# Kernel tuning notes

Hardware: AMD Instinct MI355X
Metric: run time of the kernel (lower is better)

The kernel has to match this reference:

```python
import jax, jax.numpy as jnp
import numpy as np

K = 5              # kernel_size per pseudo dim
K3 = K ** 3        # 125 kernel weight slots
BITS = np.array([[(c >> d) & 1 for d in range(3)] for c in range(8)], dtype=np.int32)  # [8,3]
STRIDES = np.array([1, K, K * K], dtype=np.int32)

N0, E0 = 16384, 262144
N1, E1 = 4096, 65536
N2, E2 = 1024, 16384
N3, E3 = 256, 4096
B = 16
V = B * 8          # final dense 2x2x2 voxels per graph


def spline_conv(x, src, dst, pseudo, W, root, bias, num_nodes):
    """Degree-1 open B-spline conv (torch SplineConv, mean aggr + root + bias).
    x: [N,in], pseudo: [E,3] in [0,1], W: [K^3,in,out]."""
    v = pseudo * (K - 1)                         # [E,3]
    lo = jnp.clip(jnp.floor(v), 0, K - 2)
    frac = v - lo                                # [E,3]
    lo = lo.astype(jnp.int32)
    bits = jnp.asarray(BITS)                     # [8,3]
    idx = lo[:, None, :] + bits[None]            # [E,8,3]
    kidx = (idx * jnp.asarray(STRIDES)).sum(-1)  # [E,8] flat kernel index
    basis = jnp.where(bits[None].astype(bool), frac[:, None, :], 1.0 - frac[:, None, :]).prod(-1)  # [E,8]
    y = jnp.einsum('ni,kio->nko', x, W)          # [N,K3,out] per-node per-kernel transform
    yv = y[src[:, None], kidx]                   # [E,8,out] gather
    msg = (basis[..., None] * yv).sum(1)         # [E,out]
    agg = jax.ops.segment_sum(msg, dst, num_segments=num_nodes)
    deg = jax.ops.segment_sum(jnp.ones(dst.shape[0], x.dtype), dst, num_segments=num_nodes)
    agg = agg / jnp.maximum(deg, 1.0)[:, None]   # mean aggregation
    return agg + x @ root + bias


def pool_max(x, cluster, num_segments):
    p = jax.ops.segment_max(x, cluster, num_segments=num_segments)
    return jnp.where(jnp.isfinite(p), p, 0.0)    # empty voxels -> 0


def setup_inputs() -> dict:
    key = jax.random.key(0)
    ks = iter(jax.random.split(key, 64))
    f = lambda s, sc: jax.random.normal(next(ks), s, jnp.float32) * sc
    u = lambda s: jax.random.uniform(next(ks), s, jnp.float32)
    ri = lambda s, hi: jax.random.randint(next(ks), s, 0, hi, dtype=jnp.int32)
    return dict(
        x0=u((N0, 1)),
        pseudo0=u((E0, 3)), pseudo1=u((E1, 3)), pseudo2=u((E2, 3)), pseudo3=u((E3, 3)),
        W1=f((K3, 1, 32), 0.3), root1=f((1, 32), 0.3), b1=f((32,), 0.05),
        W2=f((K3, 32, 64), 0.05), root2=f((32, 64), 0.05), b2=f((64,), 0.05),
        W3=f((K3, 64, 64), 0.04), root3=f((64, 64), 0.04), b3=f((64,), 0.05),
        W4=f((K3, 64, 128), 0.04), root4=f((64, 128), 0.04), b4=f((128,), 0.05),
        fc1_w=f((1024, 256), 0.03), fc1_b=f((256,), 0.05),
        fc2_w=f((256, 10), 0.06), fc2_b=f((10,), 0.05),
        src0=ri((E0,), N0), dst0=ri((E0,), N0),
        src1=ri((E1,), N1), dst1=ri((E1,), N1),
        src2=ri((E2,), N2), dst2=ri((E2,), N2),
        src3=ri((E3,), N3), dst3=ri((E3,), N3),
        cluster0=ri((N0,), N1), cluster1=ri((N1,), N2),
        cluster2=ri((N2,), N3), cluster3=ri((N3,), V),
    )


def reference(x0, pseudo0, pseudo1, pseudo2, pseudo3,
              W1, root1, b1, W2, root2, b2, W3, root3, b3, W4, root4, b4,
              fc1_w, fc1_b, fc2_w, fc2_b,
              src0, dst0, src1, dst1, src2, dst2, src3, dst3,
              cluster0, cluster1, cluster2, cluster3):
    x = jax.nn.elu(spline_conv(x0, src0, dst0, pseudo0, W1, root1, b1, N0))
    x = pool_max(x, cluster0, N1)
    x = jax.nn.elu(spline_conv(x, src1, dst1, pseudo1, W2, root2, b2, N1))
    x = pool_max(x, cluster1, N2)
    x = jax.nn.elu(spline_conv(x, src2, dst2, pseudo2, W3, root3, b3, N2))
    x = pool_max(x, cluster2, N3)
    x = jax.nn.elu(spline_conv(x, src3, dst3, pseudo3, W4, root4, b4, N3))
    x = pool_max(x, cluster3, V)                 # [B*8, 128]
    x = x.reshape(B, 8 * 128)
    x = jax.nn.elu(x @ fc1_w + fc1_b)
    x = x @ fc2_w + fc2_b                        # dropout is a no-op in eval
    return jax.nn.log_softmax(x, axis=1)
```

## Files before the change

### kernel.cpp

```cpp
#include <hip/hip_runtime.h>
#include <hip/hip_bf16.h>
#include <math.h>

namespace {

typedef unsigned long long u64;
typedef __attribute__((ext_vector_type(8))) short bf16x8;
typedef __attribute__((ext_vector_type(4))) float f32x4;

constexpr int KK = 5;
constexpr int K3 = 125;
constexpr int N0 = 16384, E0 = 262144;
constexpr int N1 = 4096,  E1 = 65536;
constexpr int N2 = 1024,  E2 = 16384;
constexpr int N3 = 256,   E3 = 4096;
constexpr int NV = 128;
constexpr int E_TOT = E0 + E1 + E2 + E3;
constexpr unsigned ENC_NEG_INF = 0x007FFFFFu;

constexpr size_t A_PENC1 = 0;
constexpr size_t A_PENC2 = A_PENC1 + (size_t)N1 * 32;
constexpr size_t A_PENC3 = A_PENC2 + (size_t)N2 * 64;
constexpr size_t A_PENC4 = A_PENC3 + (size_t)N3 * 64;
constexpr size_t A_PENC_END = A_PENC4 + (size_t)NV * 128;
constexpr size_t PENC_TOTAL = A_PENC_END;

constexpr size_t A_WT2 = A_PENC_END;
constexpr size_t A_WT3 = A_WT2 + (size_t)K3 * 64 * 32 / 2;
constexpr size_t A_WT4 = A_WT3 + (size_t)K3 * 64 * 64 / 2;

constexpr size_t A_BAS0 = A_WT4 + (size_t)K3 * 128 * 64 / 2;
constexpr size_t A_KID0 = A_BAS0 + (size_t)E0 * 8;
constexpr size_t A_BAS1 = A_KID0 + (size_t)E0 * 2;
constexpr size_t A_KID1 = A_BAS1 + (size_t)E1 * 8;
constexpr size_t A_BAS2 = A_KID1 + (size_t)E1 * 2;
constexpr size_t A_KID2 = A_BAS2 + (size_t)E2 * 8;
constexpr size_t A_BAS3 = A_KID2 + (size_t)E2 * 2;
constexpr size_t A_KID3 = A_BAS3 + (size_t)E3 * 8;

constexpr size_t A_OFF0 = A_KID3 + (size_t)E3 * 2;
constexpr size_t A_OFF1 = A_OFF0 + (N0 + 4);
constexpr size_t A_OFF2 = A_OFF1 + (N1 + 4);
constexpr size_t A_OFF3 = A_OFF2 + (N2 + 4);
constexpr size_t A_CUR0 = A_OFF3 + (N3 + 4);
constexpr size_t A_CUR1 = A_CUR0 + N0;
constexpr size_t A_CUR2 = A_CUR1 + N1;
constexpr size_t A_CUR3 = A_CUR2 + N2;
constexpr size_t A_CUR_END = A_CUR3 + N3;
constexpr size_t CUR_TOTAL = A_CUR_END - A_CUR0;
constexpr size_t A_EIX0 = A_CUR_END;
constexpr size_t A_EIX1 = A_EIX0 + E0;
constexpr size_t A_EIX2 = A_EIX1 + E1;
constexpr size_t A_EIX3 = A_EIX2 + E2;
constexpr size_t A_Y = A_EIX3 + E3;
constexpr size_t Y_FLOATS = (size_t)N1 * (K3 * 64) / 2;
constexpr size_t A_FCP = A_Y + Y_FLOATS;

__device__ __forceinline__ float eluf(float x) { return x > 0.f ? x : expm1f(x); }

__device__ __forceinline__ unsigned enc_f(float x) {
    unsigned u = __float_as_uint(x);
    return (u & 0x80000000u) ? ~u : (u | 0x80000000u);
}
__device__ __forceinline__ float dec_fin(unsigned u) {
    u = (u & 0x80000000u) ? (u & 0x7fffffffu) : ~u;
    float v = __uint_as_float(u);
    return isfinite(v) ? v : 0.f;
}
__device__ __forceinline__ float bf2f(unsigned short u) {
    return __uint_as_float((unsigned)u << 16);
}
__device__ __forceinline__ unsigned short f2bf(float v) {
    __hip_bfloat16 h = __float2bfloat16(v);
    return *reinterpret_cast<unsigned short*>(&h);
}

__device__ __forceinline__ void decode_edge(const float* __restrict__ pseudo, int e,
                                            float bas[8], int kid[8]) {
    float v0 = pseudo[e * 3 + 0] * (KK - 1);
    float v1 = pseudo[e * 3 + 1] * (KK - 1);
    float v2 = pseudo[e * 3 + 2] * (KK - 1);
    float f0 = fminf(fmaxf(floorf(v0), 0.f), (float)(KK - 2));
    float f1 = fminf(fmaxf(floorf(v1), 0.f), (float)(KK - 2));
    float f2 = fminf(fmaxf(floorf(v2), 0.f), (float)(KK - 2));
    int lo0 = (int)f0, lo1 = (int)f1, lo2 = (int)f2;
    float fr0 = v0 - f0, fr1 = v1 - f1, fr2 = v2 - f2;
#pragma unroll
    for (int c = 0; c < 8; ++c) {
        int b0 = c & 1, b1 = (c >> 1) & 1, b2 = (c >> 2) & 1;
        kid[c] = (lo0 + b0) + (lo1 + b1) * KK + (lo2 + b2) * KK * KK;
        bas[c] = (b0 ? fr0 : 1.f - fr0) * (b1 ? fr1 : 1.f - fr1) * (b2 ? fr2 : 1.f - fr2);
    }
}

__global__ void prologue1(const float* __restrict__ ps0, const float* __restrict__ ps1,
                          const float* __restrict__ ps2, const float* __restrict__ ps3,
                          const int* __restrict__ d0, const int* __restrict__ d1,
                          const int* __restrict__ d2, const int* __restrict__ d3,
                          float* __restrict__ ws) {
    int g = blockIdx.x * blockDim.x + threadIdx.x;
    if (g < (int)PENC_TOTAL) ((unsigned*)(ws + A_PENC1))[g] = ENC_NEG_INF;
    if (g >= E_TOT) return;
    const float* ps; float* bas; u64* kid; int e; const int* dst; int* cur;
    if (g < E0)                { ps = ps0; bas = ws + A_BAS0; kid = (u64*)(ws + A_KID0); e = g;                dst = d0; cur = (int*)(ws + A_CUR0); }
    else if (g < E0 + E1)      { ps = ps1; bas = ws + A_BAS1; kid = (u64*)(ws + A_KID1); e = g - E0;           dst = d1; cur = (int*)(ws + A_CUR1); }
    else if (g < E0 + E1 + E2) { ps = ps2; bas = ws + A_BAS2; kid = (u64*)(ws + A_KID2); e = g - E0 - E1;      dst = d2; cur = (int*)(ws + A_CUR2); }
    else                       { ps = ps3; bas = ws + A_BAS3; kid = (u64*)(ws + A_KID3); e = g - E0 - E1 - E2; dst = d3; cur = (int*)(ws + A_CUR3); }
    atomicAdd(&cur[dst[e]], 1);
    float b[8]; int k[8];
    decode_edge(ps, e, b, k);
    *(float4*)(bas + (size_t)e * 8)     = make_float4(b[0], b[1], b[2], b[3]);
    *(float4*)(bas + (size_t)e * 8 + 4) = make_float4(b[4], b[5], b[6], b[7]);
    u64 p = 0;
#pragma unroll
    for (int c = 0; c < 8; ++c) p |= (u64)(unsigned)k[c] << (8 * c);
    kid[e] = p;
}

__global__ void csr_scan(float* __restrict__ ws) {
    __shared__ int ls[1024];
    int* cur; int* off; int N;
    switch (blockIdx.x) {
        case 0:  cur = (int*)(ws + A_CUR0); off = (int*)(ws + A_OFF0); N = N0; break;
        case 1:  cur = (int*)(ws + A_CUR1); off = (int*)(ws + A_OFF1); N = N1; break;
        case 2:  cur = (int*)(ws + A_CUR2); off = (int*)(ws + A_OFF2); N = N2; break;
        default: cur = (int*)(ws + A_CUR3); off = (int*)(ws + A_OFF3); N = N3; break;
    }
    int t = threadIdx.x;
    int chunk = (N + 1023) >> 10;
    int b0 = t * chunk;
    int b1 = min(b0 + chunk, N);
    int s = 0;
    for (int i = b0; i < b1; ++i) s += cur[i];
    ls[t] = s;
    __syncthreads();
    for (int d = 1; d < 1024; d <<= 1) {
        int v = (t >= d) ? ls[t - d] : 0;
        __syncthreads();
        ls[t] += v;
        __syncthreads();
    }
    int run = (t == 0) ? 0 : ls[t - 1];
    for (int i = b0; i < b1; ++i) {
        int c = cur[i];
        off[i] = run;
        cur[i] = run;
        run += c;
    }
    if (t == 1023) off[N] = run;
}

__global__ void prologue4(const int* __restrict__ d0, const int* __restrict__ d1,
                          const int* __restrict__ d2, const int* __restrict__ d3,
                          const float* __restrict__ W2, const float* __restrict__ W3,
                          const float* __restrict__ W4, float* __restrict__ ws) {
    __shared__ float st[64 * 129];
    int bid = blockIdx.x;
    int tid = threadIdx.x;
    if (bid < 3 * K3) {
        const float* W; unsigned short* wt; int IN, OUT, k;
        if (bid < K3)          { W = W2; wt = (unsigned short*)(ws + A_WT2); IN = 32; OUT = 64;  k = bid; }
        else if (bid < 2 * K3) { W = W3; wt = (unsigned short*)(ws + A_WT3); IN = 64; OUT = 64;  k = bid - K3; }
        else                   { W = W4; wt = (unsigned short*)(ws + A_WT4); IN = 64; OUT = 128; k = bid - 2 * K3; }
        int tot = IN * OUT;
        const float* Wk = W + (size_t)k * tot;
        for (int idx = tid; idx < tot; idx += 256) {
            int i = idx / OUT, o = idx % OUT;
            st[i * (OUT + 1) + o] = Wk[idx];
        }
        __syncthreads();
        unsigned short* wk = wt + (size_t)k * tot;
        for (int idx = tid; idx < tot; idx += 256) {
            int o = idx / IN, i = idx % IN;
            wk[idx] = f2bf(st[i * (OUT + 1) + o]);
        }
    } else {
        int g = (bid - 3 * K3) * 256 + tid;
        if (g < E0)                { int p = atomicAdd((int*)(ws + A_CUR0) + d0[g], 1);            ((int*)(ws + A_EIX0))[p] = g; }
        else if (g < E0 + E1)      { int e = g - E0;           int p = atomicAdd((int*)(ws + A_CUR1) + d1[e], 1); ((int*)(ws + A_EIX1))[p] = e; }
        else if (g < E0 + E1 + E2) { int e = g - E0 - E1;      int p = atomicAdd((int*)(ws + A_CUR2) + d2[e], 1); ((int*)(ws + A_EIX2))[p] = e; }
        else if (g < E_TOT)        { int e = g - E0 - E1 - E2; int p = atomicAdd((int*)(ws + A_CUR3) + d3[e], 1); ((int*)(ws + A_EIX3))[p] = e; }
    }
}

__global__ __launch_bounds__(256) void l1_agg(const float* __restrict__ x0,
                                              const float* __restrict__ bas,
                                              const u64* __restrict__ kid,
                                              const int* __restrict__ src,
                                              const int* __restrict__ off,
                                              const int* __restrict__ eidx,
                                              const float* __restrict__ W1,
                                              const float* __restrict__ root1,
                                              const float* __restrict__ b1,
                                              const int* __restrict__ cl,
                                              unsigned* __restrict__ penc) {
    __shared__ float wlds[K3 * 32];
    int tid = threadIdx.x;
    for (int i = tid; i < K3 * 32; i += 256) wlds[i] = W1[i];
    __syncthreads();
    int o = tid & 31;
    int nsub = tid >> 5;
    int n = blockIdx.x * 8 + nsub;
    int s0 = off[n], s1 = off[n + 1];
    float acc = 0.f;
    int j = s0;
    for (; j + 2 <= s1; j += 2) {
        int ea = eidx[j], eb = eidx[j + 1];
        float4 qa0 = *(const float4*)(bas + (size_t)ea * 8);
        float4 qa1 = *(const float4*)(bas + (size_t)ea * 8 + 4);
        float4 qb0 = *(const float4*)(bas + (size_t)eb * 8);
        float4 qb1 = *(const float4*)(bas + (size_t)eb * 8 + 4);
        u64 ka = kid[ea], kb = kid[eb];
        float xa = x0[src[ea]], xb = x0[src[eb]];
        float ma, mb;
        ma  = qa0.x * wlds[((int)( ka        & 255u)) * 32 + o];
        ma += qa0.y * wlds[((int)((ka >>  8) & 255u)) * 32 + o];
        ma += qa0.z * wlds[((int)((ka >> 16) & 255u)) * 32 + o];
        ma += qa0.w * wlds[((int)((ka >> 24) & 255u)) * 32 + o];
        ma += qa1.x * wlds[((int)((ka >> 32) & 255u)) * 32 + o];
        ma += qa1.y * wlds[((int)((ka >> 40) & 255u)) * 32 + o];
        ma += qa1.z * wlds[((int)((ka >> 48) & 255u)) * 32 + o];
        ma += qa1.w * wlds[((int)((ka >> 56) & 255u)) * 32 + o];
        mb  = qb0.x * wlds[((int)( kb        & 255u)) * 32 + o];
        mb += qb0.y * wlds[((int)((kb >>  8) & 255u)) * 32 + o];
        mb += qb0.z * wlds[((int)((kb >> 16) & 255u)) * 32 + o];
        mb += qb0.w * wlds[((int)((kb >> 24) & 255u)) * 32 + o];
        mb += qb1.x * wlds[((int)((kb >> 32) & 255u)) * 32 + o];
        mb += qb1.y * wlds[((int)((kb >> 40) & 255u)) * 32 + o];
        mb += qb1.z * wlds[((int)((kb >> 48) & 255u)) * 32 + o];
        mb += qb1.w * wlds[((int)((kb >> 56) & 255u)) * 32 + o];
        acc = fmaf(xa, ma, fmaf(xb, mb, acc));
    }
    if (j < s1) {
        int e = eidx[j];
        float4 q0 = *(const float4*)(bas + (size_t)e * 8);
        float4 q1 = *(const float4*)(bas + (size_t)e * 8 + 4);
        u64 k8 = kid[e];
        float xv = x0[src[e]];
        float m;
        m  = q0.x * wlds[((int)( k8        & 255u)) * 32 + o];
        m += q0.y * wlds[((int)((k8 >>  8) & 255u)) * 32 + o];
        m += q0.z * wlds[((int)((k8 >> 16) & 255u)) * 32 + o];
        m += q0.w * wlds[((int)((k8 >> 24) & 255u)) * 32 + o];
        m += q1.x * wlds[((int)((k8 >> 32) & 255u)) * 32 + o];
        m += q1.y * wlds[((int)((k8 >> 40) & 255u)) * 32 + o];
        m += q1.z * wlds[((int)((k8 >> 48) & 255u)) * 32 + o];
        m += q1.w * wlds[((int)((k8 >> 56) & 255u)) * 32 + o];
        acc = fmaf(xv, m, acc);
    }
    float dg = fmaxf((float)(s1 - s0), 1.f);
    float val = acc / dg + x0[n] * root1[o] + b1[o];
    val = eluf(val);
    atomicMax(&penc[(size_t)cl[n] * 32 + o], enc_f(val));
}

template <int IN>
__global__ __launch_bounds__(256) void gemm_y_mfma(const unsigned* __restrict__ penc,
                                                   const unsigned short* __restrict__ wt,
                                                   unsigned short* __restrict__ y,
                                                   int N, int KO) {
    int wid = (blockIdx.x * 256 + threadIdx.x) >> 6;
    int lane = threadIdx.x & 63;
    int nTiles = N >> 4;
    int n0 = (wid % nTiles) << 4;
    int ko0 = (wid / nTiles) << 6;
    int l15 = lane & 15;
    int kk = (lane >> 4) << 3;

    f32x4 acc[4];
#pragma unroll
    for (int t = 0; t < 4; ++t) acc[t] = (f32x4){0.f, 0.f, 0.f, 0.f};

#pragma unroll
    for (int s = 0; s < IN / 32; ++s) {
        const unsigned* pp = penc + (size_t)(n0 + l15) * IN + s * 32 + kk;
        uint4 u0 = *(const uint4*)pp;
        uint4 u1 = *(const uint4*)(pp + 4);
        unsigned uu[8] = {u0.x, u0.y, u0.z, u0.w, u1.x, u1.y, u1.z, u1.w};
        bf16x8 bfrag;
#pragma unroll
        for (int t = 0; t < 8; ++t) bfrag[t] = (short)f2bf(dec_fin(uu[t]));
#pragma unroll
        for (int t = 0; t < 4; ++t) {
            bf16x8 afrag = *(const bf16x8*)(wt + (size_t)(ko0 + t * 16 + l15) * IN + s * 32 + kk);
            acc[t] = __builtin_amdgcn_mfma_f32_16x16x32_bf16(afrag, bfrag, acc[t], 0, 0, 0);
        }
    }
    int rbase = (lane >> 4) << 2;
#pragma unroll
    for (int t = 0; t < 4; ++t) {
        ushort4 sv;
        sv.x = f2bf(acc[t][0]);
        sv.y = f2bf(acc[t][1]);
        sv.z = f2bf(acc[t][2]);
        sv.w = f2bf(acc[t][3]);
        *(ushort4*)(y + (size_t)(n0 + l15) * KO + ko0 + t * 16 + rbase) = sv;
    }
}

template <int IN, int OUT>
__global__ __launch_bounds__(256) void gather_agg(const unsigned short* __restrict__ y,
                                                  const float* __restrict__ bas,
                                                  const u64* __restrict__ kid,
                                                  const int* __restrict__ src,
                                                  const int* __restrict__ off,
                                                  const int* __restrict__ eidx,
                                                  const unsigned* __restrict__ penc_prev,
                                                  const float* __restrict__ root,
                                                  const float* __restrict__ bias,
                                                  const int* __restrict__ cl,
                                                  unsigned* __restrict__ penc) {
    constexpr int KO = K3 * OUT;
    constexpr int WPT = OUT / 64;
    int lane = threadIdx.x & 63;
    int wv = threadIdx.x >> 6;
    int n = blockIdx.x * 4 + wv;
    int s0 = off[n], s1 = off[n + 1];
    float acc0 = 0.f, acc1 = 0.f;
    int j = s0;
    for (; j + 2 <= s1; j += 2) {
        int ea = eidx[j], eb = eidx[j + 1];
        float4 qa0 = *(const float4*)(bas + (size_t)ea * 8);
        float4 qa1 = *(const float4*)(bas + (size_t)ea * 8 + 4);
        float4 qb0 = *(const float4*)(bas + (size_t)eb * 8);
        float4 qb1 = *(const float4*)(bas + (size_t)eb * 8 + 4);
        u64 ka = kid[ea], kb = kid[eb];
        const unsigned short* ypa = y + (size_t)src[ea] * KO + lane;
        const unsigned short* ypb = y + (size_t)src[eb] * KO + lane;
        float ba[8] = {qa0.x, qa0.y, qa0.z, qa0.w, qa1.x, qa1.y, qa1.z, qa1.w};
        float bb[8] = {qb0.x, qb0.y, qb0.z, qb0.w, qb1.x, qb1.y, qb1.z, qb1.w};
        float va[8], vb[8], va2[8], vb2[8];
#pragma unroll
        for (int c = 0; c < 8; ++c) {
            int kca = (int)((ka >> (8 * c)) & 255u);
            int kcb = (int)((kb >> (8 * c)) & 255u);
            va[c] = bf2f(ypa[(size_t)kca * OUT]);
            vb[c] = bf2f(ypb[(size_t)kcb * OUT]);
            if (WPT == 2) {
                va2[c] = bf2f(ypa[(size_t)kca * OUT + 64]);
                vb2[c] = bf2f(ypb[(size_t)kcb * OUT + 64]);
            }
        }
#pragma unroll
        for (int c = 0; c < 8; ++c) {
            acc0 = fmaf(ba[c], va[c], acc0);
            acc0 = fmaf(bb[c], vb[c], acc0);
            if (WPT == 2) {
                acc1 = fmaf(ba[c], va2[c], acc1);
                acc1 = fmaf(bb[c], vb2[c], acc1);
            }
        }
    }
    if (j < s1) {
        int e = eidx[j];
        float4 q0 = *(const float4*)(bas + (size_t)e * 8);
        float4 q1 = *(const float4*)(bas + (size_t)e * 8 + 4);
        u64 k8 = kid[e];
        const unsigned short* yp = y + (size_t)src[e] * KO + lane;
        float b[8] = {q0.x, q0.y, q0.z, q0.w, q1.x, q1.y, q1.z, q1.w};
#pragma unroll
        for (int c = 0; c < 8; ++c) {
            int kc = (int)((k8 >> (8 * c)) & 255u);
            acc0 = fmaf(b[c], bf2f(yp[(size_t)kc * OUT]), acc0);
            if (WPT == 2) acc1 = fmaf(b[c], bf2f(yp[(size_t)kc * OUT + 64]), acc1);
        }
    }
    float dg = fmaxf((float)(s1 - s0), 1.f);
    float accs[2] = {acc0, acc1};
#pragma unroll
    for (int w = 0; w < WPT; ++w) {
        int o = lane + 64 * w;
        float r = 0.f;
        for (int i = 0; i < IN; ++i)
            r = fmaf(dec_fin(penc_prev[(size_t)n * IN + i]), root[(size_t)i * OUT + o], r);
        float val = accs[w] / dg + r + bias[o];
        val = eluf(val);
        atomicMax(&penc[(size_t)cl[n] * OUT + o], enc_f(val));
    }
}

__global__ __launch_bounds__(256) void fc1_part(const unsigned* __restrict__ penc4,
                                                const float* __restrict__ w1,
                                                float* __restrict__ part) {
    __shared__ float xs[64];
    int ks = blockIdx.x & 15;
    int bq = blockIdx.x >> 4;
    int t = threadIdx.x;
    int k0 = ks * 64;
    if (t < 64) xs[t] = dec_fin(penc4[(size_t)bq * 1024 + k0 + t]);
    __syncthreads();
    const float* wp = w1 + (size_t)k0 * 256 + t;
    float acc = 0.f;
#pragma unroll 8
    for (int k = 0; k < 64; ++k)
        acc = fmaf(xs[k], wp[(size_t)k * 256], acc);
    part[((size_t)bq * 16 + ks) * 256 + t] = acc;
}

__global__ __launch_bounds__(256) void fc_head2(const float* __restrict__ part,
                                                const float* __restrict__ b1,
                                                const float* __restrict__ w2,
                                                const float* __restrict__ b2,
                                                float* __restrict__ out) {
    __shared__ float h[256];
    __shared__ float l[10];
    __shared__ float red[2];
    int bq = blockIdx.x;
    int t = threadIdx.x;
    const float* pp = part + (size_t)bq * 16 * 256 + t;
    float acc = b1[t];
#pragma unroll
    for (int ks = 0; ks < 16; ++ks) acc += pp[ks * 256];
    h[t] = eluf(acc);
    __syncthreads();
    if (t < 10) {
        float a2 = b2[t];
        for (int q = 0; q < 256; ++q)
            a2 = fmaf(h[q], w2[(size_t)q * 10 + t], a2);
        l[t] = a2;
    }
    __syncthreads();
    if (t == 0) {
        float m = l[0];
        for (int i = 1; i < 10; ++i) m = fmaxf(m, l[i]);
        float s = 0.f;
        for (int i = 0; i < 10; ++i) s += expf(l[i] - m);
        red[0] = m;
        red[1] = logf(s);
    }
    __syncthreads();
    if (t < 10) out[(size_t)bq * 10 + t] = l[t] - red[0] - red[1];
}

inline unsigned blk(long long t) { return (unsigned)((t + 255) / 256); }

}

extern "C" void kernel_launch(void* const* d_in, const int* in_sizes, int n_in,
                              void* d_out, int out_size, void* d_ws, size_t ws_size,
                              hipStream_t stream) {
    const float* x0    = (const float*)d_in[0];
    const float* ps0   = (const float*)d_in[1];
    const float* ps1   = (const float*)d_in[2];
    const float* ps2   = (const float*)d_in[3];
    const float* ps3   = (const float*)d_in[4];
    const float* W1    = (const float*)d_in[5];
    const float* root1 = (const float*)d_in[6];
    const float* b1    = (const float*)d_in[7];
    const float* W2    = (const float*)d_in[8];
    const float* root2 = (const float*)d_in[9];
    const float* b2    = (const float*)d_in[10];
    const float* W3    = (const float*)d_in[11];
    const float* root3 = (const float*)d_in[12];
    const float* b3    = (const float*)d_in[13];
    const float* W4    = (const float*)d_in[14];
    const float* root4 = (const float*)d_in[15];
    const float* b4    = (const float*)d_in[16];
    const float* fc1w  = (const float*)d_in[17];
    const float* fc1b  = (const float*)d_in[18];
    const float* fc2w  = (const float*)d_in[19];
    const float* fc2b  = (const float*)d_in[20];
    const int* src0 = (const int*)d_in[21];
    const int* dst0 = (const int*)d_in[22];
    const int* src1 = (const int*)d_in[23];
    const int* dst1 = (const int*)d_in[24];
    const int* src2 = (const int*)d_in[25];
    const int* dst2 = (const int*)d_in[26];
    const int* src3 = (const int*)d_in[27];
    const int* dst3 = (const int*)d_in[28];
    const int* cl0  = (const int*)d_in[29];
    const int* cl1  = (const int*)d_in[30];
    const int* cl2  = (const int*)d_in[31];
    const int* cl3  = (const int*)d_in[32];

    float* ws = (float*)d_ws;
    float* out = (float*)d_out;

    unsigned* penc1 = (unsigned*)(ws + A_PENC1);
    unsigned* penc2 = (unsigned*)(ws + A_PENC2);
    unsigned* penc3 = (unsigned*)(ws + A_PENC3);
    unsigned* penc4 = (unsigned*)(ws + A_PENC4);
    unsigned short* wt2 = (unsigned short*)(ws + A_WT2);
    unsigned short* wt3 = (unsigned short*)(ws + A_WT3);
    unsigned short* wt4 = (unsigned short*)(ws + A_WT4);
    float* bas0 = ws + A_BAS0;  u64* kid0 = (u64*)(ws + A_KID0);
    float* bas1 = ws + A_BAS1;  u64* kid1 = (u64*)(ws + A_KID1);
    float* bas2 = ws + A_BAS2;  u64* kid2 = (u64*)(ws + A_KID2);
    float* bas3 = ws + A_BAS3;  u64* kid3 = (u64*)(ws + A_KID3);
    int* off0 = (int*)(ws + A_OFF0);  int* eix0 = (int*)(ws + A_EIX0);
    int* off1 = (int*)(ws + A_OFF1);  int* eix1 = (int*)(ws + A_EIX1);
    int* off2 = (int*)(ws + A_OFF2);  int* eix2 = (int*)(ws + A_EIX2);
    int* off3 = (int*)(ws + A_OFF3);  int* eix3 = (int*)(ws + A_EIX3);
    unsigned short* yb = (unsigned short*)(ws + A_Y);
    float* fcp = ws + A_FCP;

    hipMemsetAsync(ws + A_CUR0, 0, CUR_TOTAL * sizeof(int), stream);
    prologue1<<<blk(E_TOT), 256, 0, stream>>>(ps0, ps1, ps2, ps3, dst0, dst1, dst2, dst3, ws);
    csr_scan<<<4, 1024, 0, stream>>>(ws);
    prologue4<<<3 * K3 + blk(E_TOT), 256, 0, stream>>>(dst0, dst1, dst2, dst3, W2, W3, W4, ws);

    l1_agg<<<N0 / 8, 256, 0, stream>>>(x0, bas0, kid0, src0, off0, eix0, W1, root1, b1, cl0, penc1);

    gemm_y_mfma<32><<<(N1 / 16) * (K3 * 64 / 64) / 4, 256, 0, stream>>>(penc1, wt2, yb, N1, K3 * 64);
    gather_agg<32, 64><<<N1 / 4, 256, 0, stream>>>(yb, bas1, kid1, src1, off1, eix1,
                                                   penc1, root2, b2, cl1, penc2);

    gemm_y_mfma<64><<<(N2 / 16) * (K3 * 64 / 64) / 4, 256, 0, stream>>>(penc2, wt3, yb, N2, K3 * 64);
    gather_agg<64, 64><<<N2 / 4, 256, 0, stream>>>(yb, bas2, kid2, src2, off2, eix2,
                                                   penc2, root3, b3, cl2, penc3);

    gemm_y_mfma<64><<<(N3 / 16) * (K3 * 128 / 64) / 4, 256, 0, stream>>>(penc3, wt4, yb, N3, K3 * 128);
    gather_agg<64, 128><<<N3 / 4, 256, 0, stream>>>(yb, bas3, kid3, src3, off3, eix3,
                                                    penc3, root4, b4, cl3, penc4);

    fc1_part<<<16 * 16, 256, 0, stream>>>(penc4, fc1w, fcp);
    fc_head2<<<16, 256, 0, stream>>>(fcp, fc1b, fc2w, fc2b, out);
}
```

Measured before the change: 346.8 us.

## Fuse all phases into one persistent cooperative kernel with grid syncs

Replaces the chain of a dozen separate kernel launches with a single cooperative persistent kernel that runs every phase in grid-stride loops, separated by grid-wide barriers, and keeps the multi-launch path as a fallback. It also shrinks the CSR scan to 256 threads and splits the weight transpose into 32-row halves so one shared buffer serves all phases. The aim is to remove per-launch overhead and the gaps between dependent small kernels. In exchange, the grid is capped by occupancy, so large phases get fewer blocks and each grid.sync adds its own cost.

```diff
diff --git a/kernel.cpp b/kernel.cpp
--- a/kernel.cpp
+++ b/kernel.cpp
@@ -1,6 +1,9 @@
 #include <hip/hip_runtime.h>
+#include <hip/hip_cooperative_groups.h>
 #include <hip/hip_bf16.h>
 #include <math.h>
+
+namespace cg = cooperative_groups;
 
 namespace {
 
@@ -14,15 +17,15 @@
 constexpr int N1 = 4096,  E1 = 65536;
 constexpr int N2 = 1024,  E2 = 16384;
 constexpr int N3 = 256,   E3 = 4096;
-constexpr int NV = 128;
 constexpr int E_TOT = E0 + E1 + E2 + E3;
 constexpr unsigned ENC_NEG_INF = 0x007FFFFFu;
+constexpr int KO2 = K3 * 64, KO3 = K3 * 64, KO4 = K3 * 128;
 
 constexpr size_t A_PENC1 = 0;
 constexpr size_t A_PENC2 = A_PENC1 + (size_t)N1 * 32;
 constexpr size_t A_PENC3 = A_PENC2 + (size_t)N2 * 64;
 constexpr size_t A_PENC4 = A_PENC3 + (size_t)N3 * 64;
-constexpr size_t A_PENC_END = A_PENC4 + (size_t)NV * 128;
+constexpr size_t A_PENC_END = A_PENC4 + (size_t)128 * 128;
 constexpr size_t PENC_TOTAL = A_PENC_END;
 
 constexpr size_t A_WT2 = A_PENC_END;
@@ -53,8 +56,20 @@
 constexpr size_t A_EIX2 = A_EIX1 + E1;
 constexpr size_t A_EIX3 = A_EIX2 + E2;
 constexpr size_t A_Y = A_EIX3 + E3;
-constexpr size_t Y_FLOATS = (size_t)N1 * (K3 * 64) / 2;
+constexpr size_t Y_FLOATS = (size_t)N1 * KO2 / 2;
 constexpr size_t A_FCP = A_Y + Y_FLOATS;
+
+constexpr int SMEM_FLOATS = 4128;
+
+struct P {
+    const float *x0, *W1, *root1, *b1, *root2, *b2, *root3, *b3, *root4, *b4;
+    const float *ps0, *ps1, *ps2, *ps3;
+    const float *W2, *W3, *W4, *fc1w, *fc1b, *fc2w, *fc2b;
+    const int *src0, *dst0, *src1, *dst1, *src2, *dst2, *src3, *dst3;
+    const int *cl0, *cl1, *cl2, *cl3;
+    float* ws;
+    float* out;
+};
 
 __device__ __forceinline__ float eluf(float x) { return x > 0.f ? x : expm1f(x); }
 
@@ -93,426 +108,488 @@
     }
 }
 
-__global__ void prologue1(const float* __restrict__ ps0, const float* __restrict__ ps1,
-                          const float* __restrict__ ps2, const float* __restrict__ ps3,
-                          const int* __restrict__ d0, const int* __restrict__ d1,
-                          const int* __restrict__ d2, const int* __restrict__ d3,
-                          float* __restrict__ ws) {
-    int g = blockIdx.x * blockDim.x + threadIdx.x;
-    if (g < (int)PENC_TOTAL) ((unsigned*)(ws + A_PENC1))[g] = ENC_NEG_INF;
-    if (g >= E_TOT) return;
-    const float* ps; float* bas; u64* kid; int e; const int* dst; int* cur;
-    if (g < E0)                { ps = ps0; bas = ws + A_BAS0; kid = (u64*)(ws + A_KID0); e = g;                dst = d0; cur = (int*)(ws + A_CUR0); }
-    else if (g < E0 + E1)      { ps = ps1; bas = ws + A_BAS1; kid = (u64*)(ws + A_KID1); e = g - E0;           dst = d1; cur = (int*)(ws + A_CUR1); }
-    else if (g < E0 + E1 + E2) { ps = ps2; bas = ws + A_BAS2; kid = (u64*)(ws + A_KID2); e = g - E0 - E1;      dst = d2; cur = (int*)(ws + A_CUR2); }
-    else                       { ps = ps3; bas = ws + A_BAS3; kid = (u64*)(ws + A_KID3); e = g - E0 - E1 - E2; dst = d3; cur = (int*)(ws + A_CUR3); }
-    atomicAdd(&cur[dst[e]], 1);
-    float b[8]; int k[8];
-    decode_edge(ps, e, b, k);
-    *(float4*)(bas + (size_t)e * 8)     = make_float4(b[0], b[1], b[2], b[3]);
-    *(float4*)(bas + (size_t)e * 8 + 4) = make_float4(b[4], b[5], b[6], b[7]);
-    u64 p = 0;
-#pragma unroll
-    for (int c = 0; c < 8; ++c) p |= (u64)(unsigned)k[c] << (8 * c);
-    kid[e] = p;
-}
-
-__global__ void csr_scan(float* __restrict__ ws) {
-    __shared__ int ls[1024];
-    int* cur; int* off; int N;
-    switch (blockIdx.x) {
-        case 0:  cur = (int*)(ws + A_CUR0); off = (int*)(ws + A_OFF0); N = N0; break;
-        case 1:  cur = (int*)(ws + A_CUR1); off = (int*)(ws + A_OFF1); N = N1; break;
-        case 2:  cur = (int*)(ws + A_CUR2); off = (int*)(ws + A_OFF2); N = N2; break;
-        default: cur = (int*)(ws + A_CUR3); off = (int*)(ws + A_OFF3); N = N3; break;
-    }
-    int t = threadIdx.x;
-    int chunk = (N + 1023) >> 10;
-    int b0 = t * chunk;
-    int b1 = min(b0 + chunk, N);
-    int s = 0;
-    for (int i = b0; i < b1; ++i) s += cur[i];
-    ls[t] = s;
+__device__ void ph0(const P& p) {
+    float* ws = p.ws;
+    for (int g = blockIdx.x * 256 + threadIdx.x; g < E_TOT; g += gridDim.x * 256) {
+        if (g < (int)PENC_TOTAL) ((unsigned*)(ws + A_PENC1))[g] = ENC_NEG_INF;
+        const float* ps; float* bas; u64* kid; int e; const int* dst; int* cur;
+        if (g < E0)                { ps = p.ps0; bas = ws + A_BAS0; kid = (u64*)(ws + A_KID0); e = g;                dst = p.dst0; cur = (int*)(ws + A_CUR0); }
+        else if (g < E0 + E1)      { ps = p.ps1; bas = ws + A_BAS1; kid = (u64*)(ws + A_KID1); e = g - E0;           dst = p.dst1; cur = (int*)(ws + A_CUR1); }
+        else if (g < E0 + E1 + E2) { ps = p.ps2; bas = ws + A_BAS2; kid = (u64*)(ws + A_KID2); e = g - E0 - E1;      dst = p.dst2; cur = (int*)(ws + A_CUR2); }
+        else                       { ps = p.ps3; bas = ws + A_BAS3; kid = (u64*)(ws + A_KID3); e = g - E0 - E1 - E2; dst = p.dst3; cur = (int*)(ws + A_CUR3); }
+        atomicAdd(&cur[dst[e]], 1);
+        float b[8]; int k[8];
+        decode_edge(ps, e, b, k);
+        *(float4*)(bas + (size_t)e * 8)     = make_float4(b[0], b[1], b[2], b[3]);
+        *(float4*)(bas + (size_t)e * 8 + 4) = make_float4(b[4], b[5], b[6], b[7]);
+        u64 pk = 0;
+#pragma unroll
+        for (int c = 0; c < 8; ++c) pk |= (u64)(unsigned)k[c] << (8 * c);
+        kid[e] = pk;
+    }
+}
+
+__device__ void ph1(const P& p, float* smem) {
+    float* ws = p.ws;
+    if (blockIdx.x < 4) {
+        int* ls = (int*)smem;
+        int* cur; int* off; int N;
+        switch (blockIdx.x) {
+            case 0:  cur = (int*)(ws + A_CUR0); off = (int*)(ws + A_OFF0); N = N0; break;
+            case 1:  cur = (int*)(ws + A_CUR1); off = (int*)(ws + A_OFF1); N = N1; break;
+            case 2:  cur = (int*)(ws + A_CUR2); off = (int*)(ws + A_OFF2); N = N2; break;
+            default: cur = (int*)(ws + A_CUR3); off = (int*)(ws + A_OFF3); N = N3; break;
+        }
+        int t = threadIdx.x;
+        int chunk = N >> 8;
+        int b0 = t * chunk, b1 = b0 + chunk;
+        int s = 0;
+        for (int i = b0; i < b1; ++i) s += cur[i];
+        ls[t] = s;
+        __syncthreads();
+        for (int d = 1; d < 256; d <<= 1) {
+            int v = (t >= d) ? ls[t - d] : 0;
+            __syncthreads();
+            ls[t] += v;
+            __syncthreads();
+        }
+        int run = (t == 0) ? 0 : ls[t - 1];
+        for (int i = b0; i < b1; ++i) {
+            int c = cur[i];
+            off[i] = run;
+            cur[i] = run;
+            run += c;
+        }
+        if (t == 255) off[N] = run;
+    }
+}
+
+__device__ void ph2(const P& p, float* smem) {
+    float* ws = p.ws;
+    constexpr int NW = 3 * K3;
+    constexpr int NS = E_TOT / 256;
+    for (int u = blockIdx.x; u < NW + NS; u += gridDim.x) {
+        if (u < NW) {
+            const float* W; unsigned short* wt; int IN, OUT, k;
+            if (u < K3)          { W = p.W2; wt = (unsigned short*)(ws + A_WT2); IN = 32; OUT = 64;  k = u; }
+            else if (u < 2 * K3) { W = p.W3; wt = (unsigned short*)(ws + A_WT3); IN = 64; OUT = 64;  k = u - K3; }
+            else                 { W = p.W4; wt = (unsigned short*)(ws + A_WT4); IN = 64; OUT = 128; k = u - 2 * K3; }
+            const float* Wk = W + (size_t)k * IN * OUT;
+            unsigned short* wk = wt + (size_t)k * IN * OUT;
+            int halves = IN / 32;
+            for (int h = 0; h < halves; ++h) {
+                __syncthreads();
+                for (int idx = threadIdx.x; idx < 32 * OUT; idx += 256) {
+                    int i2 = idx / OUT, o = idx % OUT;
+                    smem[i2 * (OUT + 1) + o] = Wk[(size_t)(h * 32 + i2) * OUT + o];
+                }
+                __syncthreads();
+                for (int idx = threadIdx.x; idx < OUT * 32; idx += 256) {
+                    int o = idx / 32, i2 = idx % 32;
+                    wk[(size_t)o * IN + h * 32 + i2] = f2bf(smem[i2 * (OUT + 1) + o]);
+                }
+            }
+        } else {
+            int g = (u - NW) * 256 + threadIdx.x;
+            if (g < E0)                { int q = atomicAdd((int*)(ws + A_CUR0) + p.dst0[g], 1);            ((int*)(ws + A_EIX0))[q] = g; }
+            else if (g < E0 + E1)      { int e = g - E0;           int q = atomicAdd((int*)(ws + A_CUR1) + p.dst1[e], 1); ((int*)(ws + A_EIX1))[q] = e; }
+            else if (g < E0 + E1 + E2) { int e = g - E0 - E1;      int q = atomicAdd((int*)(ws + A_CUR2) + p.dst2[e], 1); ((int*)(ws + A_EIX2))[q] = e; }
+            else                       { int e = g - E0 - E1 - E2; int q = atomicAdd((int*)(ws + A_CUR3) + p.dst3[e], 1); ((int*)(ws + A_EIX3))[q] = e; }
+        }
+    }
+}
+
+__device__ void ph3(const P& p, float* smem) {
+    float* ws = p.ws;
+    float* wlds = smem;
+    for (int i = threadIdx.x; i < K3 * 32; i += 256) wlds[i] = p.W1[i];
     __syncthreads();
-    for (int d = 1; d < 1024; d <<= 1) {
-        int v = (t >= d) ? ls[t - d] : 0;
-        __syncthreads();
-        ls[t] += v;
-        __syncthreads();
-    }
-    int run = (t == 0) ? 0 : ls[t - 1];
-    for (int i = b0; i < b1; ++i) {
-        int c = cur[i];
-        off[i] = run;
-        cur[i] = run;
-        run += c;
-    }
-    if (t == 1023) off[N] = run;
-}
-
-__global__ void prologue4(const int* __restrict__ d0, const int* __restrict__ d1,
-                          const int* __restrict__ d2, const int* __restrict__ d3,
-                          const float* __restrict__ W2, const float* __restrict__ W3,
-                          const float* __restrict__ W4, float* __restrict__ ws) {
-    __shared__ float st[64 * 129];
-    int bid = blockIdx.x;
-    int tid = threadIdx.x;
-    if (bid < 3 * K3) {
-        const float* W; unsigned short* wt; int IN, OUT, k;
-        if (bid < K3)          { W = W2; wt = (unsigned short*)(ws + A_WT2); IN = 32; OUT = 64;  k = bid; }
-        else if (bid < 2 * K3) { W = W3; wt = (unsigned short*)(ws + A_WT3); IN = 64; OUT = 64;  k = bid - K3; }
-        else                   { W = W4; wt = (unsigned short*)(ws + A_WT4); IN = 64; OUT = 128; k = bid - 2 * K3; }
-        int tot = IN * OUT;
-        const float* Wk = W + (size_t)k * tot;
-        for (int idx = tid; idx < tot; idx += 256) {
-            int i = idx / OUT, o = idx % OUT;
-            st[i * (OUT + 1) + o] = Wk[idx];
-        }
-        __syncthreads();
-        unsigned short* wk = wt + (size_t)k * tot;
-        for (int idx = tid; idx < tot; idx += 256) {
-            int o = idx / IN, i = idx % IN;
-            wk[idx] = f2bf(st[i * (OUT + 1) + o]);
-        }
-    } else {
-        int g = (bid - 3 * K3) * 256 + tid;
-        if (g < E0)                { int p = atomicAdd((int*)(ws + A_CUR0) + d0[g], 1);            ((int*)(ws + A_EIX0))[p] = g; }
-        else if (g < E0 + E1)      { int e = g - E0;           int p = atomicAdd((int*)(ws + A_CUR1) + d1[e], 1); ((int*)(ws + A_EIX1))[p] = e; }
-        else if (g < E0 + E1 + E2) { int e = g - E0 - E1;      int p = atomicAdd((int*)(ws + A_CUR2) + d2[e], 1); ((int*)(ws + A_EIX2))[p] = e; }
-        else if (g < E_TOT)        { int e = g - E0 - E1 - E2; int p = atomicAdd((int*)(ws + A_CUR3) + d3[e], 1); ((int*)(ws + A_EIX3))[p] = e; }
-    }
-}
-
-__global__ __launch_bounds__(256) void l1_agg(const float* __restrict__ x0,
-                                              const float* __restrict__ bas,
-                                              const u64* __restrict__ kid,
-                                              const int* __restrict__ src,
-                                              const int* __restrict__ off,
-                                              const int* __restrict__ eidx,
-                                              const float* __restrict__ W1,
-                                              const float* __restrict__ root1,
-                                              const float* __restrict__ b1,
-                                              const int* __restrict__ cl,
-                                              unsigned* __restrict__ penc) {
-    __shared__ float wlds[K3 * 32];
-    int tid = threadIdx.x;
-    for (int i = tid; i < K3 * 32; i += 256) wlds[i] = W1[i];
-    __syncthreads();
-    int o = tid & 31;
-    int nsub = tid >> 5;
-    int n = blockIdx.x * 8 + nsub;
-    int s0 = off[n], s1 = off[n + 1];
-    float acc = 0.f;
-    int j = s0;
-    for (; j + 2 <= s1; j += 2) {
-        int ea = eidx[j], eb = eidx[j + 1];
-        float4 qa0 = *(const float4*)(bas + (size_t)ea * 8);
-        float4 qa1 = *(const float4*)(bas + (size_t)ea * 8 + 4);
-        float4 qb0 = *(const float4*)(bas + (size_t)eb * 8);
-        float4 qb1 = *(const float4*)(bas + (size_t)eb * 8 + 4);
-        u64 ka = kid[ea], kb = kid[eb];
-        float xa = x0[src[ea]], xb = x0[src[eb]];
-        float ma, mb;
-        ma  = qa0.x * wlds[((int)( ka        & 255u)) * 32 + o];
-        ma += qa0.y * wlds[((int)((ka >>  8) & 255u)) * 32 + o];
-        ma += qa0.z * wlds[((int)((ka >> 16) & 255u)) * 32 + o];
-        ma += qa0.w * wlds[((int)((ka >> 24) & 255u)) * 32 + o];
-        ma += qa1.x * wlds[((int)((ka >> 32) & 255u)) * 32 + o];
-        ma += qa1.y * wlds[((int)((ka >> 40) & 255u)) * 32 + o];
-        ma += qa1.z * wlds[((int)((ka >> 48) & 255u)) * 32 + o];
-        ma += qa1.w * wlds[((int)((ka >> 56) & 255u)) * 32 + o];
-        mb  = qb0.x * wlds[((int)( kb        & 255u)) * 32 + o];
-        mb += qb0.y * wlds[((int)((kb >>  8) & 255u)) * 32 + o];
-        mb += qb0.z * wlds[((int)((kb >> 16) & 255u)) * 32 + o];
-        mb += qb0.w * wlds[((int)((kb >> 24) & 255u)) * 32 + o];
-        mb += qb1.x * wlds[((int)((kb >> 32) & 255u)) * 32 + o];
-        mb += qb1.y * wlds[((int)((kb >> 40) & 255u)) * 32 + o];
-        mb += qb1.z * wlds[((int)((kb >> 48) & 255u)) * 32 + o];
-        mb += qb1.w * wlds[((int)((kb >> 56) & 255u)) * 32 + o];
-        acc = fmaf(xa, ma, fmaf(xb, mb, acc));
-    }
-    if (j < s1) {
-        int e = eidx[j];
-        float4 q0 = *(const float4*)(bas + (size_t)e * 8);
-        float4 q1 = *(const float4*)(bas + (size_t)e * 8 + 4);
-        u64 k8 = kid[e];
-        float xv = x0[src[e]];
-        float m;
-        m  = q0.x * wlds[((int)( k8        & 255u)) * 32 + o];
-        m += q0.y * wlds[((int)((k8 >>  8) & 255u)) * 32 + o];
-        m += q0.z * wlds[((int)((k8 >> 16) & 255u)) * 32 + o];
-        m += q0.w * wlds[((int)((k8 >> 24) & 255u)) * 32 + o];
-        m += q1.x * wlds[((int)((k8 >> 32) & 255u)) * 32 + o];
-        m += q1.y * wlds[((int)((k8 >> 40) & 255u)) * 32 + o];
-        m += q1.z * wlds[((int)((k8 >> 48) & 255u)) * 32 + o];
-        m += q1.w * wlds[((int)((k8 >> 56) & 255u)) * 32 + o];
-        acc = fmaf(xv, m, acc);
-    }
-    float dg = fmaxf((float)(s1 - s0), 1.f);
-    float val = acc / dg + x0[n] * root1[o] + b1[o];
-    val = eluf(val);
-    atomicMax(&penc[(size_t)cl[n] * 32 + o], enc_f(val));
+    const float* bas = ws + A_BAS0;
+    const u64* kid = (const u64*)(ws + A_KID0);
+    const int* off = (const int*)(ws + A_OFF0);
+    const int* eidx = (const int*)(ws + A_EIX0);
+    unsigned* penc = (unsigned*)(ws + A_PENC1);
+    int o = threadIdx.x & 31;
+    int nsub = threadIdx.x >> 5;
+    for (int nb = blockIdx.x; nb < N0 / 8; nb += gridDim.x) {
+        int n = nb * 8 + nsub;
+        int s0 = off[n], s1 = off[n + 1];
+        float acc = 0.f;
+        int j = s0;
+        for (; j + 2 <= s1; j += 2) {
+            int ea = eidx[j], eb = eidx[j + 1];
+            float4 qa0 = *(const float4*)(bas + (size_t)ea * 8);
+            float4 qa1 = *(const float4*)(bas + (size_t)ea * 8 + 4);
+            float4 qb0 = *(const float4*)(bas + (size_t)eb * 8);
+            float4 qb1 = *(const float4*)(bas + (size_t)eb * 8 + 4);
+            u64 ka = kid[ea], kb = kid[eb];
+            float xa = p.x0[p.src0[ea]], xb = p.x0[p.src0[eb]];
+            float ma, mb;
+            ma  = qa0.x * wlds[((int)( ka        & 255u)) * 32 + o];
+            ma += qa0.y * wlds[((int)((ka >>  8) & 255u)) * 32 + o];
+            ma += qa0.z * wlds[((int)((ka >> 16) & 255u)) * 32 + o];
+            ma += qa0.w * wlds[((int)((ka >> 24) & 255u)) * 32 + o];
+            ma += qa1.x * wlds[((int)((ka >> 32) & 255u)) * 32 + o];
+            ma += qa1.y * wlds[((int)((ka >> 40) & 255u)) * 32 + o];
+            ma += qa1.z * wlds[((int)((ka >> 48) & 255u)) * 32 + o];
+            ma += qa1.w * wlds[((int)((ka >> 56) & 255u)) * 32 + o];
+            mb  = qb0.x * wlds[((int)( kb        & 255u)) * 32 + o];
+            mb += qb0.y * wlds[((int)((kb >>  8) & 255u)) * 32 + o];
+            mb += qb0.z * wlds[((int)((kb >> 16) & 255u)) * 32 + o];
+            mb += qb0.w * wlds[((int)((kb >> 24) & 255u)) * 32 + o];
+            mb += qb1.x * wlds[((int)((kb >> 32) & 255u)) * 32 + o];
+            mb += qb1.y * wlds[((int)((kb >> 40) & 255u)) * 32 + o];
+            mb += qb1.z * wlds[((int)((kb >> 48) & 255u)) * 32 + o];
+            mb += qb1.w * wlds[((int)((kb >> 56) & 255u)) * 32 + o];
+            acc = fmaf(xa, ma, fmaf(xb, mb, acc));
+        }
+        if (j < s1) {
+            int e = eidx[j];
+            float4 q0 = *(const float4*)(bas + (size_t)e * 8);
+            float4 q1 = *(const float4*)(bas + (size_t)e * 8 + 4);
+            u64 k8 = kid[e];
+            float xv = p.x0[p.src0[e]];
+            float m;
+            m  = q0.x * wlds[((int)( k8        & 255u)) * 32 + o];
+            m += q0.y * wlds[((int)((k8 >>  8) & 255u)) * 32 + o];
+            m += q0.z * wlds[((int)((k8 >> 16) & 255u)) * 32 + o];
+            m += q0.w * wlds[((int)((k8 >> 24) & 255u)) * 32 + o];
+            m += q1.x * wlds[((int)((k8 >> 32) & 255u)) * 32 + o];
+            m += q1.y * wlds[((int)((k8 >> 40) & 255u)) * 32 + o];
+            m += q1.z * wlds[((int)((k8 >> 48) & 255u)) * 32 + o];
+            m += q1.w * wlds[((int)((k8 >> 56) & 255u)) * 32 + o];
+            acc = fmaf(xv, m, acc);
+        }
+        float dg = fmaxf((float)(s1 - s0), 1.f);
+        float val = acc / dg + p.x0[n] * p.root1[o] + p.b1[o];
+        val = eluf(val);
+        atomicMax(&penc[(size_t)p.cl0[n] * 32 + o], enc_f(val));
+    }
 }
 
 template <int IN>
-__global__ __launch_bounds__(256) void gemm_y_mfma(const unsigned* __restrict__ penc,
-                                                   const unsigned short* __restrict__ wt,
-                                                   unsigned short* __restrict__ y,
-                                                   int N, int KO) {
-    int wid = (blockIdx.x * 256 + threadIdx.x) >> 6;
+__device__ void ph_gemm(const unsigned* __restrict__ penc,
+                        const unsigned short* __restrict__ wt,
+                        unsigned short* __restrict__ y, int N, int KO) {
     int lane = threadIdx.x & 63;
+    int wsub = threadIdx.x >> 6;
     int nTiles = N >> 4;
-    int n0 = (wid % nTiles) << 4;
-    int ko0 = (wid / nTiles) << 6;
+    int totalU = nTiles * (KO / 64) / 4;
     int l15 = lane & 15;
     int kk = (lane >> 4) << 3;
-
-    f32x4 acc[4];
-#pragma unroll
-    for (int t = 0; t < 4; ++t) acc[t] = (f32x4){0.f, 0.f, 0.f, 0.f};
-
-#pragma unroll
-    for (int s = 0; s < IN / 32; ++s) {
-        const unsigned* pp = penc + (size_t)(n0 + l15) * IN + s * 32 + kk;
-        uint4 u0 = *(const uint4*)pp;
-        uint4 u1 = *(const uint4*)(pp + 4);
-        unsigned uu[8] = {u0.x, u0.y, u0.z, u0.w, u1.x, u1.y, u1.z, u1.w};
-        bf16x8 bfrag;
-#pragma unroll
-        for (int t = 0; t < 8; ++t) bfrag[t] = (short)f2bf(dec_fin(uu[t]));
+    int rbase = (lane >> 4) << 2;
+    for (int u = blockIdx.x; u < totalU; u += gridDim.x) {
+        int wid = u * 4 + wsub;
+        int n0 = (wid % nTiles) << 4;
+        int ko0 = (wid / nTiles) << 6;
+        f32x4 acc[4];
+#pragma unroll
+        for (int t = 0; t < 4; ++t) acc[t] = (f32x4){0.f, 0.f, 0.f, 0.f};
+#pragma unroll
+        for (int s = 0; s < IN / 32; ++s) {
+            const unsigned* pp = penc + (size_t)(n0 + l15) * IN + s * 32 + kk;
+            uint4 u0 = *(const uint4*)pp;
+            uint4 u1 = *(const uint4*)(pp + 4);
+            unsigned uu[8] = {u0.x, u0.y, u0.z, u0.w, u1.x, u1.y, u1.z, u1.w};
+            bf16x8 bfrag;
+#pragma unroll
+            for (int t = 0; t < 8; ++t) bfrag[t] = (short)f2bf(dec_fin(uu[t]));
+#pragma unroll
+            for (int t = 0; t < 4; ++t) {
+                bf16x8 afrag = *(const bf16x8*)(wt + (size_t)(ko0 + t * 16 + l15) * IN + s * 32 + kk);
+                acc[t] = __builtin_amdgcn_mfma_f32_16x16x32_bf16(afrag, bfrag, acc[t], 0, 0, 0);
+            }
+        }
 #pragma unroll
         for (int t = 0; t < 4; ++t) {
-            bf16x8 afrag = *(const bf16x8*)(wt + (size_t)(ko0 + t * 16 + l15) * IN + s * 32 + kk);
-            acc[t] = __builtin_amdgcn_mfma_f32_16x16x32_bf16(afrag, bfrag, acc[t], 0, 0, 0);
-        }
-    }
-    int rbase = (lane >> 4) << 2;
-#pragma unroll
-    for (int t = 0; t < 4; ++t) {
-        ushort4 sv;
-        sv.x = f2bf(acc[t][0]);
-        sv.y = f2bf(acc[t][1]);
-        sv.z = f2bf(acc[t][2]);
-        sv.w = f2bf(acc[t][3]);
-        *(ushort4*)(y + (size_t)(n0 + l15) * KO + ko0 + t * 16 + rbase) = sv;
+            ushort4 sv;
+            sv.x = f2bf(acc[t][0]);
+            sv.y = f2bf(acc[t][1]);
+            sv.z = f2bf(acc[t][2]);
+            sv.w = f2bf(acc[t][3]);
+            *(ushort4*)(y + (size_t)(n0 + l15) * KO + ko0 + t * 16 + rbase) = sv;
+        }
     }
 }
 
 template <int IN, int OUT>
-__global__ __launch_bounds__(256) void gather_agg(const unsigned short* __restrict__ y,
-                                                  const float* __restrict__ bas,
-                                                  const u64* __restrict__ kid,
-                                                  const int* __restrict__ src,
-                                                  const int* __restrict__ off,
-                                                  const int* __restrict__ eidx,
-                                                  const unsigned* __restrict__ penc_prev,
-                                                  const float* __restrict__ root,
-                                                  const float* __restrict__ bias,
-                                                  const int* __restrict__ cl,
-                                                  unsigned* __restrict__ penc) {
+__device__ void ph_gather(const unsigned short* __restrict__ y,
+                          const float* __restrict__ bas,
+                          const u64* __restrict__ kid,
+                          const int* __restrict__ src,
+                          const int* __restrict__ off,
+                          const int* __restrict__ eidx,
+                          const unsigned* __restrict__ penc_prev,
+                          const float* __restrict__ root,
+                          const float* __restrict__ bias,
+                          const int* __restrict__ cl,
+                          unsigned* __restrict__ penc, int N) {
     constexpr int KO = K3 * OUT;
     constexpr int WPT = OUT / 64;
     int lane = threadIdx.x & 63;
     int wv = threadIdx.x >> 6;
-    int n = blockIdx.x * 4 + wv;
-    int s0 = off[n], s1 = off[n + 1];
-    float acc0 = 0.f, acc1 = 0.f;
-    int j = s0;
-    for (; j + 2 <= s1; j += 2) {
-        int ea = eidx[j], eb = eidx[j + 1];
-        float4 qa0 = *(const float4*)(bas + (size_t)ea * 8);
-        float4 qa1 = *(const float4*)(bas + (size_t)ea * 8 + 4);
-        float4 qb0 = *(const float4*)(bas + (size_t)eb * 8);
-        float4 qb1 = *(const float4*)(bas + (size_t)eb * 8 + 4);
-        u64 ka = kid[ea], kb = kid[eb];
-        const unsigned short* ypa = y + (size_t)src[ea] * KO + lane;
-        const unsigned short* ypb = y + (size_t)src[eb] * KO + lane;
-        float ba[8] = {qa0.x, qa0.y, qa0.z, qa0.w, qa1.x, qa1.y, qa1.z, qa1.w};
-        float bb[8] = {qb0.x, qb0.y, qb0.z, qb0.w, qb1.x, qb1.y, qb1.z, qb1.w};
-        float va[8], vb[8], va2[8], vb2[8];
-#pragma unroll
-        for (int c = 0; c < 8; ++c) {
-            int kca = (int)((ka >> (8 * c)) & 255u);
-            int kcb = (int)((kb >> (8 * c)) & 255u);
-            va[c] = bf2f(ypa[(size_t)kca * OUT]);
-            vb[c] = bf2f(ypb[(size_t)kcb * OUT]);
-            if (WPT == 2) {
-                va2[c] = bf2f(ypa[(size_t)kca * OUT + 64]);
-                vb2[c] = bf2f(ypb[(size_t)kcb * OUT + 64]);
+    for (int u = blockIdx.x; u < N / 4; u += gridDim.x) {
+        int n = u * 4 + wv;
+        int s0 = off[n], s1 = off[n + 1];
+        float acc0 = 0.f, acc1 = 0.f;
+        int j = s0;
+        for (; j + 2 <= s1; j += 2) {
+            int ea = eidx[j], eb = eidx[j + 1];
+            float4 qa0 = *(const float4*)(bas + (size_t)ea * 8);
+            float4 qa1 = *(const float4*)(bas + (size_t)ea * 8 + 4);
+            float4 qb0 = *(const float4*)(bas + (size_t)eb * 8);
+            float4 qb1 = *(const float4*)(bas + (size_t)eb * 8 + 4);
+            u64 ka = kid[ea], kb = kid[eb];
+            const unsigned short* ypa = y + (size_t)src[ea] * KO + lane;
+            const unsigned short* ypb = y + (size_t)src[eb] * KO + lane;
+            float ba[8] = {qa0.x, qa0.y, qa0.z, qa0.w, qa1.x, qa1.y, qa1.z, qa1.w};
+            float bb[8] = {qb0.x, qb0.y, qb0.z, qb0.w, qb1.x, qb1.y, qb1.z, qb1.w};
+            float va[8], vb[8], va2[8], vb2[8];
+#pragma unroll
+            for (int c = 0; c < 8; ++c) {
+                int kca = (int)((ka >> (8 * c)) & 255u);
+                int kcb = (int)((kb >> (8 * c)) & 255u);
+                va[c] = bf2f(ypa[(size_t)kca * OUT]);
+                vb[c] = bf2f(ypb[(size_t)kcb * OUT]);
+                if (WPT == 2) {
+                    va2[c] = bf2f(ypa[(size_t)kca * OUT + 64]);
+                    vb2[c] = bf2f(ypb[(size_t)kcb * OUT + 64]);
+                }
             }
-        }
-#pragma unroll
-        for (int c = 0; c < 8; ++c) {
-            acc0 = fmaf(ba[c], va[c], acc0);
-            acc0 = fmaf(bb[c], vb[c], acc0);
-            if (WPT == 2) {
-                acc1 = fmaf(ba[c], va2[c], acc1);
-                acc1 = fmaf(bb[c], vb2[c], acc1);
+#pragma unroll
+            for (int c = 0; c < 8; ++c) {
+                acc0 = fmaf(ba[c], va[c], acc0);
+                acc0 = fmaf(bb[c], vb[c], acc0);
+                if (WPT == 2) {
+                    acc1 = fmaf(ba[c], va2[c], acc1);
+                    acc1 = fmaf(bb[c], vb2[c], acc1);
+                }
             }
         }
-    }
-    if (j < s1) {
-        int e = eidx[j];
-        float4 q0 = *(const float4*)(bas + (size_t)e * 8);
-        float4 q1 = *(const float4*)(bas + (size_t)e * 8 + 4);
-        u64 k8 = kid[e];
-        const unsigned short* yp = y + (size_t)src[e] * KO + lane;
-        float b[8] = {q0.x, q0.y, q0.z, q0.w, q1.x, q1.y, q1.z, q1.w};
-#pragma unroll
-        for (int c = 0; c < 8; ++c) {
-            int kc = (int)((k8 >> (8 * c)) & 255u);
-            acc0 = fmaf(b[c], bf2f(yp[(size_t)kc * OUT]), acc0);
-            if (WPT == 2) acc1 = fmaf(b[c], bf2f(yp[(size_t)kc * OUT + 64]), acc1);
-        }
-    }
-    float dg = fmaxf((float)(s1 - s0), 1.f);
-    float accs[2] = {acc0, acc1};
-#pragma unroll
-    for (int w = 0; w < WPT; ++w) {
-        int o = lane + 64 * w;
-        float r = 0.f;
-        for (int i = 0; i < IN; ++i)
-            r = fmaf(dec_fin(penc_prev[(size_t)n * IN + i]), root[(size_t)i * OUT + o], r);
-        float val = accs[w] / dg + r + bias[o];
-        val = eluf(val);
-        atomicMax(&penc[(size_t)cl[n] * OUT + o], enc_f(val));
-    }
-}
-
-__global__ __launch_bounds__(256) void fc1_part(const unsigned* __restrict__ penc4,
-                                                const float* __restrict__ w1,
-                                                float* __restrict__ part) {
-    __shared__ float xs[64];
-    int ks = blockIdx.x & 15;
-    int bq = blockIdx.x >> 4;
-    int t = threadIdx.x;
-    int k0 = ks * 64;
-    if (t < 64) xs[t] = dec_fin(penc4[(size_t)bq * 1024 + k0 + t]);
-    __syncthreads();
-    const float* wp = w1 + (size_t)k0 * 256 + t;
-    float acc = 0.f;
+        if (j < s1) {
+            int e = eidx[j];
+            float4 q0 = *(const float4*)(bas + (size_t)e * 8);
+            float4 q1 = *(const float4*)(bas + (size_t)e * 8 + 4);
+            u64 k8 = kid[e];
+            const unsigned short* yp = y + (size_t)src[e] * KO + lane;
+            float b[8] = {q0.x, q0.y, q0.z, q0.w, q1.x, q1.y, q1.z, q1.w};
+#pragma unroll
+            for (int c = 0; c < 8; ++c) {
+                int kc = (int)((k8 >> (8 * c)) & 255u);
+                acc0 = fmaf(b[c], bf2f(yp[(size_t)kc * OUT]), acc0);
+                if (WPT == 2) acc1 = fmaf(b[c], bf2f(yp[(size_t)kc * OUT + 64]), acc1);
+            }
+        }
+        float dg = fmaxf((float)(s1 - s0), 1.f);
+        float accs[2] = {acc0, acc1};
+#pragma unroll
+        for (int w = 0; w < WPT; ++w) {
+            int o = lane + 64 * w;
+            float r = 0.f;
+            for (int i = 0; i < IN; ++i)
+                r = fmaf(dec_fin(penc_prev[(size_t)n * IN + i]), root[(size_t)i * OUT + o], r);
+            float val = accs[w] / dg + r + bias[o];
+            val = eluf(val);
+            atomicMax(&penc[(size_t)cl[n] * OUT + o], enc_f(val));
+        }
+    }
+}
+
+__device__ void ph10(const P& p, float* smem) {
+    float* ws = p.ws;
+    const unsigned* penc4 = (const unsigned*)(ws + A_PENC4);
+    float* part = ws + A_FCP;
+    for (int u = blockIdx.x; u < 256; u += gridDim.x) {
+        __syncthreads();
+        int ks = u & 15, bq = u >> 4;
+        int t = threadIdx.x;
+        if (t < 64) smem[t] = dec_fin(penc4[(size_t)bq * 1024 + ks * 64 + t]);
+        __syncthreads();
+        const float* wp = p.fc1w + (size_t)(ks * 64) * 256 + t;
+        float acc = 0.f;
 #pragma unroll 8
-    for (int k = 0; k < 64; ++k)
-        acc = fmaf(xs[k], wp[(size_t)k * 256], acc);
-    part[((size_t)bq * 16 + ks) * 256 + t] = acc;
-}
-
-__global__ __launch_bounds__(256) void fc_head2(const float* __restrict__ part,
-                                                const float* __restrict__ b1,
-                                                const float* __restrict__ w2,
-                                                const float* __restrict__ b2,
-                                                float* __restrict__ out) {
-    __shared__ float h[256];
-    __shared__ float l[10];
-    __shared__ float red[2];
-    int bq = blockIdx.x;
-    int t = threadIdx.x;
-    const float* pp = part + (size_t)bq * 16 * 256 + t;
-    float acc = b1[t];
-#pragma unroll
-    for (int ks = 0; ks < 16; ++ks) acc += pp[ks * 256];
-    h[t] = eluf(acc);
-    __syncthreads();
-    if (t < 10) {
-        float a2 = b2[t];
-        for (int q = 0; q < 256; ++q)
-            a2 = fmaf(h[q], w2[(size_t)q * 10 + t], a2);
-        l[t] = a2;
-    }
-    __syncthreads();
-    if (t == 0) {
-        float m = l[0];
-        for (int i = 1; i < 10; ++i) m = fmaxf(m, l[i]);
-        float s = 0.f;
-        for (int i = 0; i < 10; ++i) s += expf(l[i] - m);
-        red[0] = m;
-        red[1] = logf(s);
-    }
-    __syncthreads();
-    if (t < 10) out[(size_t)bq * 10 + t] = l[t] - red[0] - red[1];
-}
-
-inline unsigned blk(long long t) { return (unsigned)((t + 255) / 256); }
-
-}
-
-extern "C" void kernel_launch(void* const* d_in, const int* in_sizes, int n_in,
-                              void* d_out, int out_size, void* d_ws, size_t ws_size,
-                              hipStream_t stream) {
-    const float* x0    = (const float*)d_in[0];
-    const float* ps0   = (const float*)d_in[1];
-    const float* ps1   = (const float*)d_in[2];
-    const float* ps2   = (const float*)d_in[3];
-    const float* ps3   = (const float*)d_in[4];
-    const float* W1    = (const float*)d_in[5];
-    const float* root1 = (const float*)d_in[6];
-    const float* b1    = (const float*)d_in[7];
-    const float* W2    = (const float*)d_in[8];
-    const float* root2 = (const float*)d_in[9];
-    const float* b2    = (const float*)d_in[10];
-    const float* W3    = (const float*)d_in[11];
-    const float* root3 = (const float*)d_in[12];
-    const float* b3    = (const float*)d_in[13];
-    const float* W4    = (const float*)d_in[14];
-    const float* root4 = (const float*)d_in[15];
-    const float* b4    = (const float*)d_in[16];
-    const float* fc1w  = (const float*)d_in[17];
-    const float* fc1b  = (const float*)d_in[18];
-    const float* fc2w  = (const float*)d_in[19];
-    const float* fc2b  = (const float*)d_in[20];
-    const int* src0 = (const int*)d_in[21];
-    const int* dst0 = (const int*)d_in[22];
-    const int* src1 = (const int*)d_in[23];
-    const int* dst1 = (const int*)d_in[24];
-    const int* src2 = (const int*)d_in[25];
-    const int* dst2 = (const int*)d_in[26];
-    const int* src3 = (const int*)d_in[27];
-    const int* dst3 = (const int*)d_in[28];
-    const int* cl0  = (const int*)d_in[29];
-    const int* cl1  = (const int*)d_in[30];
-    const int* cl2  = (const int*)d_in[31];
-    const int* cl3  = (const int*)d_in[32];
-
-    float* ws = (float*)d_ws;
-    float* out = (float*)d_out;
-
+        for (int k = 0; k < 64; ++k)
+            acc = fmaf(smem[k], wp[(size_t)k * 256], acc);
+        part[((size_t)bq * 16 + ks) * 256 + t] = acc;
+    }
+}
+
+__device__ void ph11(const P& p, float* smem) {
+    float* ws = p.ws;
+    const float* part = ws + A_FCP;
+    float* h = smem;
+    float* l = smem + 256;
+    float* red = smem + 266;
+    for (int u = blockIdx.x; u < 16; u += gridDim.x) {
+        __syncthreads();
+        int t = threadIdx.x;
+        const float* pp = part + (size_t)u * 16 * 256 + t;
+        float acc = p.fc1b[t];
+#pragma unroll
+        for (int ks = 0; ks < 16; ++ks) acc += pp[ks * 256];
+        h[t] = eluf(acc);
+        __syncthreads();
+        if (t < 10) {
+            float a2 = p.fc2b[t];
+            for (int q = 0; q < 256; ++q)
+                a2 = fmaf(h[q], p.fc2w[(size_t)q * 10 + t], a2);
+            l[t] = a2;
+        }
+        __syncthreads();
+        if (t == 0) {
+            float m = l[0];
+            for (int i = 1; i < 10; ++i) m = fmaxf(m, l[i]);
+            float s = 0.f;
+            for (int i = 0; i < 10; ++i) s += expf(l[i] - m);
+            red[0] = m;
+            red[1] = logf(s);
+        }
+        __syncthreads();
+        if (t < 10) p.out[(size_t)u * 10 + t] = l[t] - red[0] - red[1];
+    }
+}
+
+__global__ __launch_bounds__(256, 4) void mega(P p) {
+    __shared__ float smem[SMEM_FLOATS];
+    cg::grid_group grid = cg::this_grid();
+    float* ws = p.ws;
     unsigned* penc1 = (unsigned*)(ws + A_PENC1);
     unsigned* penc2 = (unsigned*)(ws + A_PENC2);
     unsigned* penc3 = (unsigned*)(ws + A_PENC3);
     unsigned* penc4 = (unsigned*)(ws + A_PENC4);
-    unsigned short* wt2 = (unsigned short*)(ws + A_WT2);
-    unsigned short* wt3 = (unsigned short*)(ws + A_WT3);
-    unsigned short* wt4 = (unsigned short*)(ws + A_WT4);
-    float* bas0 = ws + A_BAS0;  u64* kid0 = (u64*)(ws + A_KID0);
-    float* bas1 = ws + A_BAS1;  u64* kid1 = (u64*)(ws + A_KID1);
-    float* bas2 = ws + A_BAS2;  u64* kid2 = (u64*)(ws + A_KID2);
-    float* bas3 = ws + A_BAS3;  u64* kid3 = (u64*)(ws + A_KID3);
-    int* off0 = (int*)(ws + A_OFF0);  int* eix0 = (int*)(ws + A_EIX0);
-    int* off1 = (int*)(ws + A_OFF1);  int* eix1 = (int*)(ws + A_EIX1);
-    int* off2 = (int*)(ws + A_OFF2);  int* eix2 = (int*)(ws + A_EIX2);
-    int* off3 = (int*)(ws + A_OFF3);  int* eix3 = (int*)(ws + A_EIX3);
     unsigned short* yb = (unsigned short*)(ws + A_Y);
-    float* fcp = ws + A_FCP;
-
-    hipMemsetAsync(ws + A_CUR0, 0, CUR_TOTAL * sizeof(int), stream);
-    prologue1<<<blk(E_TOT), 256, 0, stream>>>(ps0, ps1, ps2, ps3, dst0, dst1, dst2, dst3, ws);
-    csr_scan<<<4, 1024, 0, stream>>>(ws);
-    prologue4<<<3 * K3 + blk(E_TOT), 256, 0, stream>>>(dst0, dst1, dst2, dst3, W2, W3, W4, ws);
-
-    l1_agg<<<N0 / 8, 256, 0, stream>>>(x0, bas0, kid0, src0, off0, eix0, W1, root1, b1, cl0, penc1);
-
-    gemm_y_mfma<32><<<(N1 / 16) * (K3 * 64 / 64) / 4, 256, 0, stream>>>(penc1, wt2, yb, N1, K3 * 64);
-    gather_agg<32, 64><<<N1 / 4, 256, 0, stream>>>(yb, bas1, kid1, src1, off1, eix1,
-                                                   penc1, root2, b2, cl1, penc2);
-
-    gemm_y_mfma<64><<<(N2 / 16) * (K3 * 64 / 64) / 4, 256, 0, stream>>>(penc2, wt3, yb, N2, K3 * 64);
-    gather_agg<64, 64><<<N2 / 4, 256, 0, stream>>>(yb, bas2, kid2, src2, off2, eix2,
-                                                   penc2, root3, b3, cl2, penc3);
-
-    gemm_y_mfma<64><<<(N3 / 16) * (K3 * 128 / 64) / 4, 256, 0, stream>>>(penc3, wt4, yb, N3, K3 * 128);
-    gather_agg<64, 128><<<N3 / 4, 256, 0, stream>>>(yb, bas3, kid3, src3, off3, eix3,
-                                                    penc3, root4, b4, cl3, penc4);
-
-    fc1_part<<<16 * 16, 256, 0, stream>>>(penc4, fc1w, fcp);
-    fc_head2<<<16, 256, 0, stream>>>(fcp, fc1b, fc2w, fc2b, out);
-}
+
+    ph0(p);                     grid.sync();
+    ph1(p, smem);               grid.sync();
+    ph2(p, smem);               grid.sync();
+    ph3(p, smem);               grid.sync();
+    ph_gemm<32>(penc1, (unsigned short*)(ws + A_WT2), yb, N1, KO2);  grid.sync();
+    ph_gather<32, 64>(yb, ws + A_BAS1, (u64*)(ws + A_KID1), p.src1,
+                      (int*)(ws + A_OFF1), (int*)(ws + A_EIX1),
+                      penc1, p.root2, p.b2, p.cl1, penc2, N1);       grid.sync();
+    ph_gemm<64>(penc2, (unsigned short*)(ws + A_WT3), yb, N2, KO3);  grid.sync();
+    ph_gather<64, 64>(yb, ws + A_BAS2, (u64*)(ws + A_KID2), p.src2,
+                      (int*)(ws + A_OFF2), (int*)(ws + A_EIX2),
+                      penc2, p.root3, p.b3, p.cl2, penc3, N2);       grid.sync();
+    ph_gemm<64>(penc3, (unsigned short*)(ws + A_WT4), yb, N3, KO4);  grid.sync();
+    ph_gather<64, 128>(yb, ws + A_BAS3, (u64*)(ws + A_KID3), p.src3,
+                       (int*)(ws + A_OFF3), (int*)(ws + A_EIX3),
+                       penc3, p.root4, p.b4, p.cl3, penc4, N3);      grid.sync();
+    ph10(p, smem);              grid.sync();
+    ph11(p, smem);
+}
+
+__global__ __launch_bounds__(256) void k_ph0(P p)  { ph0(p); }
+__global__ __launch_bounds__(256) void k_ph1(P p)  { __shared__ float s[SMEM_FLOATS]; ph1(p, s); }
+__global__ __launch_bounds__(256) void k_ph2(P p)  { __shared__ float s[SMEM_FLOATS]; ph2(p, s); }
+__global__ __launch_bounds__(256) void k_ph3(P p)  { __shared__ float s[SMEM_FLOATS]; ph3(p, s); }
+__global__ __launch_bounds__(256) void k_gemm2(P p) {
+    ph_gemm<32>((unsigned*)(p.ws + A_PENC1), (unsigned short*)(p.ws + A_WT2),
+                (unsigned short*)(p.ws + A_Y), N1, KO2);
+}
+__global__ __launch_bounds__(256) void k_gath2(P p) {
+    ph_gather<32, 64>((unsigned short*)(p.ws + A_Y), p.ws + A_BAS1, (u64*)(p.ws + A_KID1), p.src1,
+                      (int*)(p.ws + A_OFF1), (int*)(p.ws + A_EIX1),
+                      (unsigned*)(p.ws + A_PENC1), p.root2, p.b2, p.cl1,
+                      (unsigned*)(p.ws + A_PENC2), N1);
+}
+__global__ __launch_bounds__(256) void k_gemm3(P p) {
+    ph_gemm<64>((unsigned*)(p.ws + A_PENC2), (unsigned short*)(p.ws + A_WT3),
+                (unsigned short*)(p.ws + A_Y), N2, KO3);
+}
+__global__ __launch_bounds__(256) void k_gath3(P p) {
+    ph_gather<64, 64>((unsigned short*)(p.ws + A_Y), p.ws + A_BAS2, (u64*)(p.ws + A_KID2), p.src2,
+                      (int*)(p.ws + A_OFF2), (int*)(p.ws + A_EIX2),
+                      (unsigned*)(p.ws + A_PENC2), p.root3, p.b3, p.cl2,
+                      (unsigned*)(p.ws + A_PENC3), N2);
+}
+__global__ __launch_bounds__(256) void k_gemm4(P p) {
+    ph_gemm<64>((unsigned*)(p.ws + A_PENC3), (unsigned short*)(p.ws + A_WT4),
+                (unsigned short*)(p.ws + A_Y), N3, KO4);
+}
+__global__ __launch_bounds__(256) void k_gath4(P p) {
+    ph_gather<64, 128>((unsigned short*)(p.ws + A_Y), p.ws + A_BAS3, (u64*)(p.ws + A_KID3), p.src3,
+                       (int*)(p.ws + A_OFF3), (int*)(p.ws + A_EIX3),
+                       (unsigned*)(p.ws + A_PENC3), p.root4, p.b4, p.cl3,
+                       (unsigned*)(p.ws + A_PENC4), N3);
+}
+__global__ __launch_bounds__(256) void k_ph10(P p) { __shared__ float s[SMEM_FLOATS]; ph10(p, s); }
+__global__ __launch_bounds__(256) void k_ph11(P p) { __shared__ float s[SMEM_FLOATS]; ph11(p, s); }
+
+}
+
+extern "C" void kernel_launch(void* const* d_in, const int* in_sizes, int n_in,
+                              void* d_out, int out_size, void* d_ws, size_t ws_size,
+                              hipStream_t stream) {
+    P p;
+    p.x0    = (const float*)d_in[0];
+    p.ps0   = (const float*)d_in[1];
+    p.ps1   = (const float*)d_in[2];
+    p.ps2   = (const float*)d_in[3];
+    p.ps3   = (const float*)d_in[4];
+    p.W1    = (const float*)d_in[5];
+    p.root1 = (const float*)d_in[6];
+    p.b1    = (const float*)d_in[7];
+    p.W2    = (const float*)d_in[8];
+    p.root2 = (const float*)d_in[9];
+    p.b2    = (const float*)d_in[10];
+    p.W3    = (const float*)d_in[11];
+    p.root3 = (const float*)d_in[12];
+    p.b3    = (const float*)d_in[13];
+    p.W4    = (const float*)d_in[14];
+    p.root4 = (const float*)d_in[15];
+    p.b4    = (const float*)d_in[16];
+    p.fc1w  = (const float*)d_in[17];
+    p.fc1b  = (const float*)d_in[18];
+    p.fc2w  = (const float*)d_in[19];
+    p.fc2b  = (const float*)d_in[20];
+    p.src0 = (const int*)d_in[21];
+    p.dst0 = (const int*)d_in[22];
+    p.src1 = (const int*)d_in[23];
+    p.dst1 = (const int*)d_in[24];
+    p.src2 = (const int*)d_in[25];
+    p.dst2 = (const int*)d_in[26];
+    p.src3 = (const int*)d_in[27];
+    p.dst3 = (const int*)d_in[28];
+    p.cl0  = (const int*)d_in[29];
+    p.cl1  = (const int*)d_in[30];
+    p.cl2  = (const int*)d_in[31];
+    p.cl3  = (const int*)d_in[32];
+    p.ws = (float*)d_ws;
+    p.out = (float*)d_out;
+
+    hipMemsetAsync(p.ws + A_CUR0, 0, CUR_TOTAL * sizeof(int), stream);
+
+    bool done = false;
+    int dev = 0;
+    if (hipGetDevice(&dev) == hipSuccess) {
+        int coop = 0, cus = 0, perCU = 0;
+        (void)hipDeviceGetAttribute(&coop, hipDeviceAttributeCooperativeLaunch, dev);
+        (void)hipDeviceGetAttribute(&cus, hipDeviceAttributeMultiprocessorCount, dev);
+        (void)hipOccupancyMaxActiveBlocksPerMultiprocessor(&perCU, mega, 256, 0);
+        if (coop && cus > 0 && perCU > 0) {
+            long long g = (long long)perCU * cus;
+            int grid = (int)(g > 2048 ? 2048 : g);
+            if (grid >= 16) {
+                void* args[] = {(void*)&p};
+                if (hipLaunchCooperativeKernel(mega, dim3(grid), dim3(256),
+                                               args, 0, stream) == hipSuccess)
+                    done = true;
+            }
+        }
+    }
+    if (!done) {
+        k_ph0<<<(E_TOT + 255) / 256, 256, 0, stream>>>(p);
+        k_ph1<<<4, 256, 0, stream>>>(p);
+        k_ph2<<<3 * K3 + E_TOT / 256, 256, 0, stream>>>(p);
+        k_ph3<<<N0 / 8, 256, 0, stream>>>(p);
+        k_gemm2<<<(N1 / 16) * (KO2 / 64) / 4, 256, 0, stream>>>(p);
+        k_gath2<<<N1 / 4, 256, 0, stream>>>(p);
+        k_gemm3<<<(N2 / 16) * (KO3 / 64) / 4, 256, 0, stream>>>(p);
+        k_gath3<<<N2 / 4, 256, 0, stream>>>(p);
+        k_gemm4<<<(N3 / 16) * (KO4 / 64) / 4, 256, 0, stream>>>(p);
+        k_gath4<<<N3 / 4, 256, 0, stream>>>(p);
+        k_ph10<<<256, 256, 0, stream>>>(p);
+        k_ph11<<<16, 256, 0, stream>>>(p);
+    }
+}
```

Measured after the change: 1.058 ms. 205% more time.
